# Performance work log

Measured on AMD Instinct MI355X. Metric: run time of the kernel, lower is better.

The kernel has to match this reference:

```python
import jax, jax.numpy as jnp
import numpy as np

B, P, T = 4, 32, 128          # batch, n_paras, n_tokens
C, TC = 16, 64                # n_clusters, n_cluster_tokens
H, NH, FF, V = 256, 8, 1024, 32000


def _ln(x, g, b, eps=1e-6):
    m = jnp.mean(x, axis=-1, keepdims=True)
    v = jnp.var(x, axis=-1, keepdims=True)
    return (x - m) / jnp.sqrt(v + eps) * g + b


def _encode(tokens, emb, pad):
    # simplified NewTransformerEncoder: token embedding as per-token context,
    # masked mean-pool as the node feature
    m = tokens != pad                       # [B, N, T]
    x = emb[tokens] * m[..., None]          # [B, N, T, H]
    denom = jnp.maximum(m.sum(-1)[..., None].astype(x.dtype), 1.0)
    feat = x.sum(2) / denom                 # [B, N, H]
    return feat, x


def _gat(q_nodes, kv_nodes, mask, wq, wk, wv, wo, nh):
    # edge-masked multi-head cross attention (MultiHeadedGAT)
    Bq, Nq, Hd = q_nodes.shape
    Nk = kv_nodes.shape[1]
    d = Hd // nh
    q = (q_nodes @ wq).reshape(Bq, Nq, nh, d)
    k = (kv_nodes @ wk).reshape(Bq, Nk, nh, d)
    v = (kv_nodes @ wv).reshape(Bq, Nk, nh, d)
    s = jnp.einsum('bqhd,bkhd->bhqk', q, k) / jnp.sqrt(jnp.asarray(d, q.dtype))
    s = jnp.where(mask[:, None, :, :], s, jnp.asarray(-1e9, s.dtype))
    a = jax.nn.softmax(s, axis=-1)
    o = jnp.einsum('bhqk,bkhd->bqhd', a, v).reshape(Bq, Nq, Hd) @ wo
    has_nb = mask.any(-1)[..., None].astype(o.dtype)  # zero out isolated nodes
    return q_nodes + o * has_nb


def _ffn(x, w1, b1, w2, b2, g, bt):
    h = jax.nn.relu(_ln(x, g, bt) @ w1 + b1)
    return h @ w2 + b2 + x


def setup_inputs() -> dict:
    key = jax.random.key(0)
    ks = jax.random.split(key, 20)
    s = 0.02
    w = lambda k, sh: (jax.random.normal(k, sh) * s).astype(jnp.float32)
    return {
        'src': jax.random.randint(ks[0], (B, P, T), 0, V),
        'cluster': jax.random.randint(ks[1], (B, C, TC), 0, V),
        'edge': jax.random.randint(ks[2], (B, P, C), 0, 2).astype(jnp.int32),
        'emb': w(ks[3], (V, H)),
        'p2c_wq': w(ks[4], (H, H)), 'p2c_wk': w(ks[5], (H, H)),
        'p2c_wv': w(ks[6], (H, H)), 'p2c_wo': w(ks[7], (H, H)),
        'c2p_wq': w(ks[8], (H, H)), 'c2p_wk': w(ks[9], (H, H)),
        'c2p_wv': w(ks[10], (H, H)), 'c2p_wo': w(ks[11], (H, H)),
        'ff_w1': w(ks[12], (H, FF)), 'ff_b1': jnp.zeros((FF,), jnp.float32),
        'ff_w2': w(ks[13], (FF, H)), 'ff_b2': jnp.zeros((H,), jnp.float32),
        'ff_ln_g': jnp.ones((H,), jnp.float32), 'ff_ln_b': jnp.zeros((H,), jnp.float32),
        'gat_iter': 2, 'padding_idx': 0, 'n_heads': NH,
    }


def reference(src, cluster, edge, emb,
              p2c_wq, p2c_wk, p2c_wv, p2c_wo,
              c2p_wq, c2p_wk, c2p_wv, c2p_wo,
              ff_w1, ff_b1, ff_w2, ff_b2, ff_ln_g, ff_ln_b,
              gat_iter, padding_idx, n_heads):
    para_feature, para_context = _encode(src, emb, padding_idx)      # [B,P,H], [B,P,T,H]
    cluster_feature, _ = _encode(cluster, emb, padding_idx)          # [B,C,H]
    e_pc = edge > 0                                                  # [B,P,C]
    e_cp = jnp.transpose(e_pc, (0, 2, 1))                            # [B,C,P]

    cluster_state = cluster_feature
    para_state = _gat(para_feature, cluster_feature, e_pc,
                      p2c_wq, p2c_wk, p2c_wv, p2c_wo, n_heads)
    for _ in range(gat_iter):
        cluster_state = _gat(cluster_state, para_state, e_cp,
                             c2p_wq, c2p_wk, c2p_wv, c2p_wo, n_heads)
        para_state = _gat(para_state, cluster_state, e_pc,
                          p2c_wq, p2c_wk, p2c_wv, p2c_wo, n_heads)

    para_context = _ffn(para_context + para_state[:, :, None, :],
                        ff_w1, ff_b1, ff_w2, ff_b2, ff_ln_g, ff_ln_b)
    mask_para = (src != padding_idx)[..., None].astype(para_context.dtype)
    para_context = para_context * mask_para
    return para_state, para_context, cluster_state
```

## Files before the change

### kernel.cpp

```cpp
#include <hip/hip_runtime.h>
#include <hip/hip_bf16.h>

#define BB 4
#define PP 32
#define TT 128
#define CC 16
#define TCC 64
#define HH 256
#define NHH 8
#define DD 32
#define FFF 1024

typedef __attribute__((ext_vector_type(8))) short bh8;
typedef __attribute__((ext_vector_type(4))) float f32x4;

__device__ float g_para_feat [BB * PP * HH];
__device__ float g_clus_feat [BB * CC * HH];
__device__ float g_para_state[BB * PP * HH];
__device__ __align__(16) short g_wp[HH * FFF + FFF * HH];
__device__ __align__(16) short g_gatw[8 * HH * HH];

__device__ __forceinline__ short f2b(float f) {
    union { __hip_bfloat16 h; short s; } u;
    u.h = __float2bfloat16(f);
    return u.s;
}
__device__ __forceinline__ float bs2f(short s) {
    union { float f; unsigned u; } x;
    x.u = ((unsigned)(unsigned short)s) << 16;
    return x.f;
}
__device__ __forceinline__ void gll16(const void* g, void* l) {
    __builtin_amdgcn_global_load_lds(
        (const __attribute__((address_space(1))) void*)g,
        (__attribute__((address_space(3))) void*)l, 16, 0, 0);
}

__global__ void __launch_bounds__(256) k_prep(
        const float* __restrict__ w1, const float* __restrict__ w2,
        const float* __restrict__ pq, const float* __restrict__ pk,
        const float* __restrict__ pv, const float* __restrict__ po,
        const float* __restrict__ cq, const float* __restrict__ ck,
        const float* __restrict__ cv, const float* __restrict__ co,
        const int* __restrict__ src, const int* __restrict__ cluster,
        const float* __restrict__ emb) {
    int tid = threadIdx.x;
    if (blockIdx.x < 256) {
        int idx = blockIdx.x * 256 + tid;
        int c = idx >> 11, wi = idx & 2047;
        int lane = wi & 63, quad = (lane >> 4) & 3, col = lane & 15;
        short* dst = g_wp + (size_t)idx * 8;
        if (wi < 1024) {
            int f = wi >> 6;
            int nt = f & 1, kk = f >> 1;
            int n = c * 32 + nt * 16 + col;
            #pragma unroll
            for (int j = 0; j < 8; j++)
                dst[j] = f2b(w1[(kk * 32 + quad * 8 + j) * FFF + n]);
        } else {
            int nt2 = (wi - 1024) >> 6;
            int n = nt2 * 16 + col;
            #pragma unroll
            for (int j = 0; j < 8; j++)
                dst[j] = f2b(w2[(c * 32 + quad * 8 + j) * HH + n]);
        }
    } else if (blockIdx.x < 448) {
        int bid = blockIdx.x - 256;
        __shared__ int stok[TT];
        if (bid < BB * PP) {
            if (tid < TT) stok[tid] = src[bid * TT + tid];
            __syncthreads();
            float acc = 0.f; int cnt = 0;
            #pragma unroll 8
            for (int i = 0; i < TT; i++) {
                int tk = stok[i];
                float e = emb[(size_t)tk * HH + tid];
                int nz = (tk != 0);
                cnt += nz; acc += nz ? e : 0.f;
            }
            g_para_feat[bid * HH + tid] = acc / fmaxf((float)cnt, 1.0f);
        } else {
            int cid = bid - BB * PP;
            if (tid < TCC) stok[tid] = cluster[cid * TCC + tid];
            __syncthreads();
            float acc = 0.f; int cnt = 0;
            #pragma unroll 8
            for (int i = 0; i < TCC; i++) {
                int tk = stok[i];
                float e = emb[(size_t)tk * HH + tid];
                int nz = (tk != 0);
                cnt += nz; acc += nz ? e : 0.f;
            }
            g_clus_feat[cid * HH + tid] = acc / fmaxf((float)cnt, 1.0f);
        }
    } else {
        int pid = blockIdx.x - 448;
        int mat = pid >> 5;
        int gi = (pid & 31) * 256 + tid;
        int lane = gi & 63, quad = (lane >> 4) & 3, col = lane & 15;
        int f = gi >> 6;
        int nt = f & 15, kk = f >> 4;
        const float* ws = (mat == 0) ? pq : (mat == 1) ? pk : (mat == 2) ? pv :
                          (mat == 3) ? po : (mat == 4) ? cq : (mat == 5) ? ck :
                          (mat == 6) ? cv : co;
        short* dst = g_gatw + ((size_t)mat * 8192 + gi) * 8;
        int n = nt * 16 + col;
        #pragma unroll
        for (int j = 0; j < 8; j++)
            dst[j] = f2b(ws[(kk * 32 + quad * 8 + j) * HH + n]);
    }
}

template<int NQ, int NK>
__device__ void gat_layer(int tid,
                          float (*__restrict__ qs)[264], short (*__restrict__ qsb)[264],
                          short (*__restrict__ kvb)[264],
                          const short* __restrict__ wm,
                          const int* __restrict__ msk, const int* __restrict__ has,
                          short (*__restrict__ s_q)[264],
                          short (*__restrict__ s_k)[264],
                          short (*__restrict__ s_vT)[44],
                          short (*__restrict__ s_pb)[32][44]) {
    constexpr int MTQ = NQ / 16, MTK = NK / 16;
    int w = tid >> 6, lane = tid & 63, quad = (lane >> 4) & 3, col = lane & 15;

    constexpr int NI1 = ((MTQ + 2 * MTK) * 16) / 16;
    #pragma unroll
    for (int it = 0; it < NI1; it++) {
        int jid = it * 16 + w;
        int nt = jid & 15, t = jid >> 4;
        int mi, mt;
        if (t < MTQ)            { mi = 0; mt = t; }
        else if (t < MTQ + MTK) { mi = 1; mt = t - MTQ; }
        else                    { mi = 2; mt = t - MTQ - MTK; }
        const short (*Ab)[264] = (mi == 0) ? qsb : kvb;
        const short* bb = wm + mi * 65536;
        bh8 Bf[8];
        #pragma unroll
        for (int kk = 0; kk < 8; kk++)
            Bf[kk] = *(const bh8*)(bb + ((kk * 16 + nt) * 64 + lane) * 8);
        f32x4 acc = (f32x4){0.f, 0.f, 0.f, 0.f};
        #pragma unroll
        for (int kk = 0; kk < 8; kk++) {
            bh8 a = *(const bh8*)&Ab[mt * 16 + col][kk * 32 + quad * 8];
            acc = __builtin_amdgcn_mfma_f32_16x16x32_bf16(a, Bf[kk], acc, 0, 0, 0);
        }
        #pragma unroll
        for (int r = 0; r < 4; r++) {
            int row = mt * 16 + quad * 4 + r, n = nt * 16 + col;
            if (mi == 0)      s_q[row][n] = f2b(acc[r]);
            else if (mi == 1) s_k[row][n] = f2b(acc[r]);
            else              s_vT[n][row] = f2b(acc[r]);
        }
    }
    if (NK == 16 && tid < 512) {
        int d = tid >> 1, o = 16 + (tid & 1) * 8;
        #pragma unroll
        for (int j = 0; j < 8; j++) s_vT[d][o + j] = 0;
    }
    __syncthreads();

    constexpr int NI2 = (8 * MTQ * MTK) / 16;
    #pragma unroll
    for (int it = 0; it < NI2; it++) {
        int jid = it * 16 + w;
        int h = jid & 7, rest = jid >> 3;
        int mt = rest % MTQ, nt = rest / MTQ;
        bh8 a  = *(const bh8*)&s_q[mt * 16 + col][h * 32 + quad * 8];
        bh8 bf = *(const bh8*)&s_k[nt * 16 + col][h * 32 + quad * 8];
        f32x4 acc = (f32x4){0.f, 0.f, 0.f, 0.f};
        acc = __builtin_amdgcn_mfma_f32_16x16x32_bf16(a, bf, acc, 0, 0, 0);
        #pragma unroll
        for (int r = 0; r < 4; r++) {
            int qrow = mt * 16 + quad * 4 + r, krow = nt * 16 + col;
            int bit = (msk[qrow] >> krow) & 1;
            s_pb[h][qrow][krow] = f2b(bit ? acc[r] * 0.17677669529663687f : -1e9f);
        }
    }
    __syncthreads();

    if (tid < NQ * 8) {
        int qi = tid >> 3, h = tid & 7;
        float av[NK]; float mx = -1e30f;
        #pragma unroll
        for (int k = 0; k < NK; k++) { av[k] = bs2f(s_pb[h][qi][k]); mx = fmaxf(mx, av[k]); }
        float sm = 0.f;
        #pragma unroll
        for (int k = 0; k < NK; k++) { av[k] = __expf(av[k] - mx); sm += av[k]; }
        float inv = 1.f / sm;
        #pragma unroll
        for (int k = 0; k < NK; k++) s_pb[h][qi][k] = f2b(av[k] * inv);
        if (NK == 16) {
            #pragma unroll
            for (int k = 16; k < 32; k++) s_pb[h][qi][k] = 0;
        }
    }
    __syncthreads();

    constexpr int NI4 = (8 * MTQ * 2) / 16;
    #pragma unroll
    for (int it = 0; it < NI4; it++) {
        int jid = it * 16 + w;
        int h = jid & 7, rest = jid >> 3;
        int mt = rest % MTQ, nt2 = rest / MTQ;
        bh8 a  = *(const bh8*)&s_pb[h][mt * 16 + col][quad * 8];
        bh8 bf = *(const bh8*)&s_vT[h * 32 + nt2 * 16 + col][quad * 8];
        f32x4 acc = (f32x4){0.f, 0.f, 0.f, 0.f};
        acc = __builtin_amdgcn_mfma_f32_16x16x32_bf16(a, bf, acc, 0, 0, 0);
        #pragma unroll
        for (int r = 0; r < 4; r++)
            s_q[mt * 16 + quad * 4 + r][h * 32 + nt2 * 16 + col] = f2b(acc[r]);
    }
    __syncthreads();

    constexpr int NI5 = (MTQ * 16) / 16;
    #pragma unroll
    for (int it = 0; it < NI5; it++) {
        int jid = it * 16 + w;
        int nt = jid & 15, mt = jid >> 4;
        const short* bb = wm + 3 * 65536;
        bh8 Bf[8];
        #pragma unroll
        for (int kk = 0; kk < 8; kk++)
            Bf[kk] = *(const bh8*)(bb + ((kk * 16 + nt) * 64 + lane) * 8);
        f32x4 acc = (f32x4){0.f, 0.f, 0.f, 0.f};
        #pragma unroll
        for (int kk = 0; kk < 8; kk++) {
            bh8 a = *(const bh8*)&s_q[mt * 16 + col][kk * 32 + quad * 8];
            acc = __builtin_amdgcn_mfma_f32_16x16x32_bf16(a, Bf[kk], acc, 0, 0, 0);
        }
        #pragma unroll
        for (int r = 0; r < 4; r++) {
            int row = mt * 16 + quad * 4 + r, n = nt * 16 + col;
            float nv = qs[row][n] + (has[row] ? acc[r] : 0.f);
            qs[row][n] = nv;
            qsb[row][n] = f2b(nv);
        }
    }
    __syncthreads();
}

__global__ void __launch_bounds__(1024, 4) k_gat(const int* __restrict__ edge,
                                                 float* __restrict__ out_ps,
                                                 float* __restrict__ out_cs) {
    __shared__ __align__(16) float s_ps [PP][264];
    __shared__ __align__(16) float s_cs [CC][264];
    __shared__ __align__(16) short s_psb[PP][264];
    __shared__ __align__(16) short s_csb[CC][264];
    __shared__ __align__(16) short s_q  [PP][264];
    __shared__ __align__(16) short s_k  [PP][264];
    __shared__ __align__(16) short s_vT [HH][44];
    __shared__ __align__(16) short s_pb [NHH][32][44];
    __shared__ int s_mskP[PP], s_hasP[PP], s_mskC[CC], s_hasC[CC];

    int b = blockIdx.x, tid = threadIdx.x;
    const int* eb = edge + b * PP * CC;

    #pragma unroll
    for (int rep = 0; rep < 8; rep++) {
        int idx = rep * 1024 + tid;
        float v = g_para_feat[b * PP * HH + idx];
        s_ps[idx >> 8][idx & 255] = v;
        s_psb[idx >> 8][idx & 255] = f2b(v);
    }
    #pragma unroll
    for (int rep = 0; rep < 4; rep++) {
        int idx = rep * 1024 + tid;
        float v = g_clus_feat[b * CC * HH + idx];
        s_cs[idx >> 8][idx & 255] = v;
        s_csb[idx >> 8][idx & 255] = f2b(v);
    }
    if (tid < PP) {
        int m = 0;
        #pragma unroll
        for (int k = 0; k < CC; k++) m |= (eb[tid * CC + k] > 0) << k;
        s_mskP[tid] = m; s_hasP[tid] = (m != 0);
    } else if (tid < PP + CC) {
        int ci = tid - PP, m = 0;
        #pragma unroll
        for (int p = 0; p < PP; p++) m |= (eb[p * CC + ci] > 0) << p;
        s_mskC[ci] = m; s_hasC[ci] = (m != 0);
    }
    __syncthreads();

    const short* wmp = g_gatw;
    const short* wmc = g_gatw + 4 * 65536;

    gat_layer<PP, CC>(tid, s_ps, s_psb, s_csb, wmp, s_mskP, s_hasP, s_q, s_k, s_vT, s_pb);
    gat_layer<CC, PP>(tid, s_cs, s_csb, s_psb, wmc, s_mskC, s_hasC, s_q, s_k, s_vT, s_pb);
    gat_layer<PP, CC>(tid, s_ps, s_psb, s_csb, wmp, s_mskP, s_hasP, s_q, s_k, s_vT, s_pb);
    gat_layer<CC, PP>(tid, s_cs, s_csb, s_psb, wmc, s_mskC, s_hasC, s_q, s_k, s_vT, s_pb);
    gat_layer<PP, CC>(tid, s_ps, s_psb, s_csb, wmp, s_mskP, s_hasP, s_q, s_k, s_vT, s_pb);

    #pragma unroll
    for (int rep = 0; rep < 8; rep++) {
        int idx = rep * 1024 + tid;
        float v = s_ps[idx >> 8][idx & 255];
        out_ps[b * PP * HH + idx] = v;
        g_para_state[b * PP * HH + idx] = v;
    }
    #pragma unroll
    for (int rep = 0; rep < 4; rep++) {
        int idx = rep * 1024 + tid;
        out_cs[b * CC * HH + idx] = s_cs[idx >> 8][idx & 255];
    }
}

__global__ void __launch_bounds__(256) k_ffn_mfma(
        const int* __restrict__ src, const float* __restrict__ emb,
        const float* __restrict__ b1, const float* __restrict__ b2v,
        const float* __restrict__ lng, const float* __restrict__ lnb,
        float* __restrict__ out_ctx) {
    __shared__ __align__(16) short xr[64][264];
    __shared__ __align__(16) short wbuf[2][16384];
    __shared__ __align__(16) short sbuf[64][40];
    __shared__ float red_s[64][4], red_s2[64][4];
    __shared__ float mu[64], rsd[64];
    __shared__ short sg[HH], sbt[HH];
    __shared__ int   toks[64];

    int tid = threadIdx.x;
    int t0 = blockIdx.x * 64;
    int pr = blockIdx.x >> 1;
    const float* psr = g_para_state + pr * HH;

    if (tid < 64) toks[tid] = src[t0 + tid];
    sg[tid]  = f2b(lng[tid]);
    sbt[tid] = f2b(lnb[tid]);
    __syncthreads();

    {
        float psv = psr[tid];
        #pragma unroll 8
        for (int m = 0; m < 64; m++) {
            int tk = toks[m];
            float e = emb[(size_t)tk * HH + tid];
            xr[m][tid] = f2b((tk ? e : 0.f) + psv);
        }
    }
    __syncthreads();
    {
        int m = tid >> 2, q = tid & 3;
        float s = 0.f, s2 = 0.f;
        #pragma unroll
        for (int jb = 0; jb < 8; jb++) {
            bh8 v8 = *(const bh8*)&xr[m][q * 64 + jb * 8];
            #pragma unroll
            for (int e = 0; e < 8; e++) { float v = bs2f(v8[e]); s += v; s2 += v * v; }
        }
        red_s[m][q] = s; red_s2[m][q] = s2;
    }
    __syncthreads();
    if (tid < 64) {
        float s  = red_s [tid][0] + red_s [tid][1] + red_s [tid][2] + red_s [tid][3];
        float s2 = red_s2[tid][0] + red_s2[tid][1] + red_s2[tid][2] + red_s2[tid][3];
        float mean = s * (1.f / HH);
        float var  = s2 * (1.f / HH) - mean * mean;
        mu[tid] = mean; rsd[tid] = rsqrtf(var + 1e-6f);
    }
    __syncthreads();

    int wv = tid >> 6, lane = tid & 63, quad = (lane >> 4) & 3, col = lane & 15;
    int sh = wv & 1, ch = wv >> 1;

    bh8 A1[2][8];
    #pragma unroll
    for (int si = 0; si < 2; si++) {
        int row = (sh * 2 + si) * 16 + col;
        float m_ = mu[row], r_ = rsd[row];
        #pragma unroll
        for (int kk = 0; kk < 8; kk++) {
            int d0 = kk * 32 + quad * 8;
            bh8 xv = *(const bh8*)&xr[row][d0];
            bh8 gv = *(const bh8*)&sg[d0];
            bh8 bv = *(const bh8*)&sbt[d0];
            bh8 o;
            #pragma unroll
            for (int e = 0; e < 8; e++)
                o[e] = f2b((bs2f(xv[e]) - m_) * r_ * bs2f(gv[e]) + bs2f(bv[e]));
            A1[si][kk] = o;
        }
    }

    {
        const char* gb = (const char*)g_wp + wv * 8192 + lane * 16;
        char* lb = (char*)&wbuf[0][0] + wv * 8192;
        #pragma unroll
        for (int i = 0; i < 8; i++)
            gll16(gb + i * 1024, lb + i * 1024);
    }

    f32x4 acc2[2][8];
    #pragma unroll
    for (int si = 0; si < 2; si++)
        #pragma unroll
        for (int j2 = 0; j2 < 8; j2++) acc2[si][j2] = (f32x4){0.f, 0.f, 0.f, 0.f};

    for (int c = 0; c < 32; c++) {
        int cur = c & 1;
        __syncthreads();

        const short* w1s = &wbuf[cur][0];
        f32x4 acc1[2];
        acc1[0] = (f32x4){0.f, 0.f, 0.f, 0.f};
        acc1[1] = (f32x4){0.f, 0.f, 0.f, 0.f};
        #pragma unroll
        for (int kk = 0; kk < 8; kk++) {
            bh8 bf = *(const bh8*)(w1s + ((kk * 2 + ch) * 64 + lane) * 8);
            acc1[0] = __builtin_amdgcn_mfma_f32_16x16x32_bf16(A1[0][kk], bf, acc1[0], 0, 0, 0);
            acc1[1] = __builtin_amdgcn_mfma_f32_16x16x32_bf16(A1[1][kk], bf, acc1[1], 0, 0, 0);
        }
        {
            float bias = b1[c * 32 + ch * 16 + col];
            #pragma unroll
            for (int si = 0; si < 2; si++)
                #pragma unroll
                for (int r = 0; r < 4; r++) {
                    float v = acc1[si][r] + bias;
                    sbuf[(sh * 2 + si) * 16 + quad * 4 + r][ch * 16 + col] =
                        f2b(v > 0.f ? v : 0.f);
                }
        }
        __syncthreads();

        if (c + 1 < 32) {
            const char* gb = (const char*)g_wp + (size_t)(c + 1) * 32768
                           + wv * 8192 + lane * 16;
            char* lb = (char*)&wbuf[1 - cur][0] + wv * 8192;
            #pragma unroll
            for (int i = 0; i < 8; i++)
                gll16(gb + i * 1024, lb + i * 1024);
        }

        const short* w2s = &wbuf[cur][0] + 8192;
        #pragma unroll
        for (int si = 0; si < 2; si++) {
            bh8 a2 = *(const bh8*)&sbuf[(sh * 2 + si) * 16 + col][quad * 8];
            #pragma unroll
            for (int j2 = 0; j2 < 8; j2++) {
                bh8 bf = *(const bh8*)(w2s + ((ch * 8 + j2) * 64 + lane) * 8);
                acc2[si][j2] = __builtin_amdgcn_mfma_f32_16x16x32_bf16(a2, bf, acc2[si][j2], 0, 0, 0);
            }
        }
    }

    #pragma unroll
    for (int j2 = 0; j2 < 8; j2++) {
        int n = (ch * 8 + j2) * 16 + col;
        float bias = b2v[n];
        #pragma unroll
        for (int si = 0; si < 2; si++)
            #pragma unroll
            for (int r = 0; r < 4; r++) {
                int ml = (sh * 2 + si) * 16 + quad * 4 + r;
                int gt = t0 + ml;
                int tk = toks[ml];
                float x = bs2f(xr[ml][n]);
                out_ctx[(size_t)gt * HH + n] = tk ? (acc2[si][j2][r] + bias + x) : 0.f;
            }
    }
}

extern "C" void kernel_launch(void* const* d_in, const int* in_sizes, int n_in,
                              void* d_out, int out_size, void* d_ws, size_t ws_size,
                              hipStream_t stream) {
    const int*   src     = (const int*)d_in[0];
    const int*   cluster = (const int*)d_in[1];
    const int*   edge    = (const int*)d_in[2];
    const float* emb     = (const float*)d_in[3];
    const float* p2c_wq  = (const float*)d_in[4];
    const float* p2c_wk  = (const float*)d_in[5];
    const float* p2c_wv  = (const float*)d_in[6];
    const float* p2c_wo  = (const float*)d_in[7];
    const float* c2p_wq  = (const float*)d_in[8];
    const float* c2p_wk  = (const float*)d_in[9];
    const float* c2p_wv  = (const float*)d_in[10];
    const float* c2p_wo  = (const float*)d_in[11];
    const float* w1      = (const float*)d_in[12];
    const float* b1      = (const float*)d_in[13];
    const float* w2      = (const float*)d_in[14];
    const float* b2p     = (const float*)d_in[15];
    const float* lng     = (const float*)d_in[16];
    const float* lnb     = (const float*)d_in[17];

    float* out      = (float*)d_out;
    float* out_ctx  = out + BB * PP * HH;
    float* out_clus = out + BB * PP * HH + BB * PP * TT * HH;

    k_prep<<<dim3(704), dim3(256), 0, stream>>>(w1, w2,
        p2c_wq, p2c_wk, p2c_wv, p2c_wo, c2p_wq, c2p_wk, c2p_wv, c2p_wo,
        src, cluster, emb);
    k_gat<<<dim3(BB), dim3(1024), 0, stream>>>(edge, out, out_clus);
    k_ffn_mfma<<<dim3(256), dim3(256), 0, stream>>>(src, emb, b1, b2p, lng, lnb, out_ctx);
}
```

Measured before the change: 217.0 us.

## Give each wave its own 16-row slice in the FFN to drop a barrier

Changes the FFN kernel's work split so each of the four waves owns 16 token rows and computes every FF column chunk and every output column for those rows, instead of splitting rows and columns two by two. The hidden activation tile then stays private to each wave in its own shared-memory slot, which removes one block-wide barrier per chunk. The cost is twice as many LDS weight reads per wave for both GEMMs, since weight fragments are no longer shared across a row-pair split, and 16 accumulator tiles per wave raise register pressure.

```diff
diff --git a/kernel.cpp b/kernel.cpp
--- a/kernel.cpp
+++ b/kernel.cpp
@@ -313,7 +313,7 @@
         float* __restrict__ out_ctx) {
     __shared__ __align__(16) short xr[64][264];
     __shared__ __align__(16) short wbuf[2][16384];
-    __shared__ __align__(16) short sbuf[64][40];
+    __shared__ __align__(16) short sbuf[4][16][40];
     __shared__ float red_s[64][4], red_s2[64][4];
     __shared__ float mu[64], rsd[64];
     __shared__ short sg[HH], sbt[HH];
@@ -361,12 +361,10 @@
     __syncthreads();
 
     int wv = tid >> 6, lane = tid & 63, quad = (lane >> 4) & 3, col = lane & 15;
-    int sh = wv & 1, ch = wv >> 1;
-
-    bh8 A1[2][8];
-    #pragma unroll
-    for (int si = 0; si < 2; si++) {
-        int row = (sh * 2 + si) * 16 + col;
+
+    bh8 A1[8];
+    {
+        int row = wv * 16 + col;
         float m_ = mu[row], r_ = rsd[row];
         #pragma unroll
         for (int kk = 0; kk < 8; kk++) {
@@ -378,7 +376,7 @@
             #pragma unroll
             for (int e = 0; e < 8; e++)
                 o[e] = f2b((bs2f(xv[e]) - m_) * r_ * bs2f(gv[e]) + bs2f(bv[e]));
-            A1[si][kk] = o;
+            A1[kk] = o;
         }
     }
 
@@ -390,37 +388,12 @@
             gll16(gb + i * 1024, lb + i * 1024);
     }
 
-    f32x4 acc2[2][8];
-    #pragma unroll
-    for (int si = 0; si < 2; si++)
-        #pragma unroll
-        for (int j2 = 0; j2 < 8; j2++) acc2[si][j2] = (f32x4){0.f, 0.f, 0.f, 0.f};
+    f32x4 acc2[16];
+    #pragma unroll
+    for (int j2 = 0; j2 < 16; j2++) acc2[j2] = (f32x4){0.f, 0.f, 0.f, 0.f};
 
     for (int c = 0; c < 32; c++) {
         int cur = c & 1;
-        __syncthreads();
-
-        const short* w1s = &wbuf[cur][0];
-        f32x4 acc1[2];
-        acc1[0] = (f32x4){0.f, 0.f, 0.f, 0.f};
-        acc1[1] = (f32x4){0.f, 0.f, 0.f, 0.f};
-        #pragma unroll
-        for (int kk = 0; kk < 8; kk++) {
-            bh8 bf = *(const bh8*)(w1s + ((kk * 2 + ch) * 64 + lane) * 8);
-            acc1[0] = __builtin_amdgcn_mfma_f32_16x16x32_bf16(A1[0][kk], bf, acc1[0], 0, 0, 0);
-            acc1[1] = __builtin_amdgcn_mfma_f32_16x16x32_bf16(A1[1][kk], bf, acc1[1], 0, 0, 0);
-        }
-        {
-            float bias = b1[c * 32 + ch * 16 + col];
-            #pragma unroll
-            for (int si = 0; si < 2; si++)
-                #pragma unroll
-                for (int r = 0; r < 4; r++) {
-                    float v = acc1[si][r] + bias;
-                    sbuf[(sh * 2 + si) * 16 + quad * 4 + r][ch * 16 + col] =
-                        f2b(v > 0.f ? v : 0.f);
-                }
-        }
         __syncthreads();
 
         if (c + 1 < 32) {
@@ -432,32 +405,50 @@
                 gll16(gb + i * 1024, lb + i * 1024);
         }
 
-        const short* w2s = &wbuf[cur][0] + 8192;
-        #pragma unroll
-        for (int si = 0; si < 2; si++) {
-            bh8 a2 = *(const bh8*)&sbuf[(sh * 2 + si) * 16 + col][quad * 8];
-            #pragma unroll
-            for (int j2 = 0; j2 < 8; j2++) {
-                bh8 bf = *(const bh8*)(w2s + ((ch * 8 + j2) * 64 + lane) * 8);
-                acc2[si][j2] = __builtin_amdgcn_mfma_f32_16x16x32_bf16(a2, bf, acc2[si][j2], 0, 0, 0);
+        const short* w1s = &wbuf[cur][0];
+        const short* w2s = w1s + 8192;
+
+        f32x4 acc1[2];
+        acc1[0] = (f32x4){0.f, 0.f, 0.f, 0.f};
+        acc1[1] = (f32x4){0.f, 0.f, 0.f, 0.f};
+        #pragma unroll
+        for (int kk = 0; kk < 8; kk++) {
+            bh8 b0 = *(const bh8*)(w1s + ((kk * 2 + 0) * 64 + lane) * 8);
+            bh8 b1f = *(const bh8*)(w1s + ((kk * 2 + 1) * 64 + lane) * 8);
+            acc1[0] = __builtin_amdgcn_mfma_f32_16x16x32_bf16(A1[kk], b0,  acc1[0], 0, 0, 0);
+            acc1[1] = __builtin_amdgcn_mfma_f32_16x16x32_bf16(A1[kk], b1f, acc1[1], 0, 0, 0);
+        }
+        {
+            float bias0 = b1[c * 32 + col];
+            float bias1 = b1[c * 32 + 16 + col];
+            #pragma unroll
+            for (int r = 0; r < 4; r++) {
+                float v0 = acc1[0][r] + bias0;
+                float v1 = acc1[1][r] + bias1;
+                sbuf[wv][quad * 4 + r][col]      = f2b(v0 > 0.f ? v0 : 0.f);
+                sbuf[wv][quad * 4 + r][16 + col] = f2b(v1 > 0.f ? v1 : 0.f);
             }
         }
-    }
-
-    #pragma unroll
-    for (int j2 = 0; j2 < 8; j2++) {
-        int n = (ch * 8 + j2) * 16 + col;
+        bh8 a2 = *(const bh8*)&sbuf[wv][col][quad * 8];
+        #pragma unroll
+        for (int nt2 = 0; nt2 < 16; nt2++) {
+            bh8 bf = *(const bh8*)(w2s + (nt2 * 64 + lane) * 8);
+            acc2[nt2] = __builtin_amdgcn_mfma_f32_16x16x32_bf16(a2, bf, acc2[nt2], 0, 0, 0);
+        }
+    }
+
+    #pragma unroll
+    for (int nt2 = 0; nt2 < 16; nt2++) {
+        int n = nt2 * 16 + col;
         float bias = b2v[n];
         #pragma unroll
-        for (int si = 0; si < 2; si++)
-            #pragma unroll
-            for (int r = 0; r < 4; r++) {
-                int ml = (sh * 2 + si) * 16 + quad * 4 + r;
-                int gt = t0 + ml;
-                int tk = toks[ml];
-                float x = bs2f(xr[ml][n]);
-                out_ctx[(size_t)gt * HH + n] = tk ? (acc2[si][j2][r] + bias + x) : 0.f;
-            }
+        for (int r = 0; r < 4; r++) {
+            int ml = wv * 16 + quad * 4 + r;
+            int gt = t0 + ml;
+            int tk = toks[ml];
+            float x = bs2f(xr[ml][n]);
+            out_ctx[(size_t)gt * HH + n] = tk ? (acc2[nt2][r] + bias + x) : 0.f;
+        }
     }
 }
 
```

After: 217.7 us. No clear change (+0.3%).
